# Performance work log

Hardware: AMD Instinct MI355X
Metric: run time of the kernel (lower is better)

The kernel has to match this reference:

```python
import jax, jax.numpy as jnp
import numpy as np

DIM = 768
HEADS = 16
DIM_HEAD = DIM // HEADS
SCALE = DIM_HEAD ** -0.5


def setup_inputs() -> dict:
    key = jax.random.key(0)
    k1, k2, k3, k4 = jax.random.split(key, 4)
    B, N = 8, 1024
    x = jax.random.normal(k1, (B, N, DIM), dtype=jnp.float32)
    # nn.Linear(dim, 3*dim, bias=False): stored so that qkv = x @ Wqkv
    Wqkv = jax.random.normal(k2, (DIM, 3 * DIM), dtype=jnp.float32) * (DIM ** -0.5)
    Wo = jax.random.normal(k3, (DIM, DIM), dtype=jnp.float32) * (DIM ** -0.5)
    bo = jax.random.normal(k4, (DIM,), dtype=jnp.float32) * 0.01
    return {"x": x, "Wqkv": Wqkv, "Wo": Wo, "bo": bo}


def reference(x, Wqkv, Wo, bo):
    B, N, _ = x.shape
    qkv = x @ Wqkv                                   # [B, N, 3*dim]
    # Faithful to torch: qkv.view(3, B, h, N, dim_head) — raw memory reshape
    qkv = jnp.reshape(qkv, (3, B, HEADS, N, DIM_HEAD))
    q, k, v = qkv[0], qkv[1], qkv[2]                 # each [B, h, N, dh]
    attn = jnp.einsum('bhnd,bhmd->bhnm', q, k) * SCALE   # [B, h, N, N]
    weight = jax.nn.softmax(attn, axis=-1)
    context = jnp.einsum('bhnm,bhmd->bhnd', weight, v)   # [B, h, N, dh]
    # Faithful to torch: context.view(B, -1, dim) — raw memory reshape
    concat = jnp.reshape(context, (B, N, DIM))
    return concat @ Wo + bo                          # dropout is identity at eval
```

## Files before the change

### kernel.cpp

```cpp
#include <hip/hip_runtime.h>
#include <hip/hip_bf16.h>

typedef __bf16 bf16x8 __attribute__((ext_vector_type(8)));
typedef __bf16 bf16x4 __attribute__((ext_vector_type(4)));
typedef float  f32x4  __attribute__((ext_vector_type(4)));

#define C2LOG 0.20823509f

__device__ __forceinline__ void gload_lds16(const __bf16* g, __bf16* l) {
    __builtin_amdgcn_global_load_lds(
        (const __attribute__((address_space(1))) void*)g,
        (__attribute__((address_space(3))) void*)l,
        16, 0, 0);
}

__global__ __launch_bounds__(256)
void prepass_kernel(const float* __restrict__ x, const float* __restrict__ Wqkv,
                    const float* __restrict__ Wo, __bf16* __restrict__ Xbf,
                    __bf16* __restrict__ WqkvT, __bf16* __restrict__ WoT) {
    __shared__ float tile[32][33];
    const int bx = blockIdx.x, t = threadIdx.x;
    if (bx < 6144) {
        const int i = (bx * 256 + t) * 4;
        float4 v = *(const float4*)&x[i];
        bf16x4 o;
        o[0] = (__bf16)v.x; o[1] = (__bf16)v.y; o[2] = (__bf16)v.z; o[3] = (__bf16)v.w;
        *(bf16x4*)&Xbf[i] = o;
        return;
    }
    const float* in; __bf16* out; int R, C, bxx;
    if (bx < 6144 + 1728) { bxx = bx - 6144; in = Wqkv; out = WqkvT; R = 768; C = 2304;
        const int c0 = (bxx % 72) * 32, r0 = (bxx / 72) * 32;
        const int tx = t & 31, ty = t >> 5;
#pragma unroll
        for (int i = 0; i < 4; ++i)
            tile[ty + i * 8][tx] = in[(size_t)(r0 + ty + i * 8) * C + c0 + tx];
        __syncthreads();
#pragma unroll
        for (int i = 0; i < 4; ++i)
            out[(size_t)(c0 + ty + i * 8) * R + r0 + tx] = (__bf16)tile[tx][ty + i * 8];
    } else { bxx = bx - 6144 - 1728; in = Wo; out = WoT; R = 768; C = 768;
        const int c0 = (bxx % 24) * 32, r0 = (bxx / 24) * 32;
        const int tx = t & 31, ty = t >> 5;
#pragma unroll
        for (int i = 0; i < 4; ++i)
            tile[ty + i * 8][tx] = in[(size_t)(r0 + ty + i * 8) * C + c0 + tx];
        __syncthreads();
#pragma unroll
        for (int i = 0; i < 4; ++i)
            out[(size_t)(c0 + ty + i * 8) * R + r0 + tx] = (__bf16)tile[tx][ty + i * 8];
    }
}

__global__ __launch_bounds__(256, 3)
void gemm_bt_kernel(const __bf16* __restrict__ A, const __bf16* __restrict__ B,
                    __bf16* __restrict__ C, int M, int N, int K) {
    __shared__ __bf16 sA[128 * 64];
    __shared__ __bf16 sB[128 * 64];

    const int m0 = blockIdx.y * 128;
    const int n0 = blockIdx.x * 128;
    const int t = threadIdx.x;
    const int w = t >> 6, lane = t & 63;
    const int quad = lane >> 4, l15 = lane & 15;
    const int wm = w >> 1, wn = w & 1;

    int aRow[4], aKc[4];
#pragma unroll
    for (int b = 0; b < 4; ++b) {
        const int L = b * 256 + t;
        aRow[b] = L >> 3;
        aKc[b] = (L & 7) ^ (aRow[b] & 7);
    }

    f32x4 acc[4][4] = {};

    for (int k0 = 0; k0 < K; k0 += 64) {
#pragma unroll
        for (int b = 0; b < 4; ++b) {
            const int ldsOff = (b * 256 + w * 64) * 8;
            gload_lds16(A + (size_t)(m0 + aRow[b]) * K + k0 + aKc[b] * 8, &sA[ldsOff]);
            gload_lds16(B + (size_t)(n0 + aRow[b]) * K + k0 + aKc[b] * 8, &sB[ldsOff]);
        }
        __syncthreads();

#pragma unroll
        for (int ks = 0; ks < 2; ++ks) {
            bf16x8 aF[4], bF[4];
            const int slot = ((ks * 4 + quad) ^ (l15 & 7)) * 8;
#pragma unroll
            for (int mt = 0; mt < 4; ++mt)
                aF[mt] = *(const bf16x8*)&sA[(wm * 64 + mt * 16 + l15) * 64 + slot];
#pragma unroll
            for (int nt = 0; nt < 4; ++nt)
                bF[nt] = *(const bf16x8*)&sB[(wn * 64 + nt * 16 + l15) * 64 + slot];
#pragma unroll
            for (int mt = 0; mt < 4; ++mt)
#pragma unroll
                for (int nt = 0; nt < 4; ++nt)
                    acc[mt][nt] = __builtin_amdgcn_mfma_f32_16x16x32_bf16(aF[mt], bF[nt], acc[mt][nt], 0, 0, 0);
        }
        __syncthreads();
    }

#pragma unroll
    for (int nt = 0; nt < 4; ++nt) {
        const int col = n0 + wn * 64 + nt * 16 + l15;
#pragma unroll
        for (int mt = 0; mt < 4; ++mt)
#pragma unroll
            for (int r = 0; r < 4; ++r) {
                const int row = m0 + wm * 64 + mt * 16 + quad * 4 + r;
                C[(size_t)row * N + col] = (__bf16)acc[mt][nt][r];
            }
    }
}

__global__ __launch_bounds__(256, 4)
void gemm_bt64_kernel(const __bf16* __restrict__ A, const __bf16* __restrict__ B,
                      float* __restrict__ C, const float* __restrict__ bias,
                      int M, int N, int K) {
    __shared__ __bf16 sA[128 * 64];
    __shared__ __bf16 sB[64 * 64];

    const int m0 = blockIdx.y * 128;
    const int n0 = blockIdx.x * 64;
    const int t = threadIdx.x;
    const int w = t >> 6, lane = t & 63;
    const int quad = lane >> 4, l15 = lane & 15;

    int sRow[4], sKc[4];
#pragma unroll
    for (int b = 0; b < 4; ++b) {
        const int L = b * 256 + t;
        sRow[b] = L >> 3;
        sKc[b] = (L & 7) ^ (sRow[b] & 7);
    }

    f32x4 acc[2][4] = {};

    for (int k0 = 0; k0 < K; k0 += 64) {
#pragma unroll
        for (int b = 0; b < 4; ++b)
            gload_lds16(A + (size_t)(m0 + sRow[b]) * K + k0 + sKc[b] * 8,
                        &sA[(b * 256 + w * 64) * 8]);
#pragma unroll
        for (int b = 0; b < 2; ++b)
            gload_lds16(B + (size_t)(n0 + sRow[b]) * K + k0 + sKc[b] * 8,
                        &sB[(b * 256 + w * 64) * 8]);
        __syncthreads();

#pragma unroll
        for (int ks = 0; ks < 2; ++ks) {
            bf16x8 aF[2], bF[4];
            const int slot = ((ks * 4 + quad) ^ (l15 & 7)) * 8;
#pragma unroll
            for (int mt = 0; mt < 2; ++mt)
                aF[mt] = *(const bf16x8*)&sA[(w * 32 + mt * 16 + l15) * 64 + slot];
#pragma unroll
            for (int nt = 0; nt < 4; ++nt)
                bF[nt] = *(const bf16x8*)&sB[(nt * 16 + l15) * 64 + slot];
#pragma unroll
            for (int mt = 0; mt < 2; ++mt)
#pragma unroll
                for (int nt = 0; nt < 4; ++nt)
                    acc[mt][nt] = __builtin_amdgcn_mfma_f32_16x16x32_bf16(aF[mt], bF[nt], acc[mt][nt], 0, 0, 0);
        }
        __syncthreads();
    }

#pragma unroll
    for (int nt = 0; nt < 4; ++nt) {
        const int col = n0 + nt * 16 + l15;
        const float bv = bias[col];
#pragma unroll
        for (int mt = 0; mt < 2; ++mt)
#pragma unroll
            for (int r = 0; r < 4; ++r) {
                const int row = m0 + w * 32 + mt * 16 + quad * 4 + r;
                C[(size_t)row * N + col] = acc[mt][nt][r] + bv;
            }
    }
}

#define VT_STRIDE 132
#define P_STRIDE  132

__global__ __launch_bounds__(512, 4)
void attn_kernel(const __bf16* __restrict__ Y1, __bf16* __restrict__ Ctx) {
    __shared__ __bf16 Kl[128 * 64];
    __shared__ __bf16 Vt[48 * VT_STRIDE];
    __shared__ __bf16 Pl[128 * P_STRIDE];

    const int bx = blockIdx.x;
    const int bh = bx & 127, qt = bx >> 7;
    const int t = threadIdx.x, w = t >> 6, lane = t & 63;
    const int quad = lane >> 4, l15 = lane & 15;

    const size_t qBase = (size_t)bh * 49152;
    const size_t kBase = 6291456 + qBase;
    const size_t vBase = 12582912 + qBase;

    bf16x8 qf0, qf1;
    {
        const int row = qt * 128 + w * 16 + l15;
        qf0 = *(const bf16x8*)(Y1 + qBase + (size_t)row * 48 + quad * 8);
        if (quad < 2)
            qf1 = *(const bf16x8*)(Y1 + qBase + (size_t)row * 48 + 32 + quad * 8);
        else
            qf1 = bf16x8{};
    }

    const int kr0 = t >> 3, kd0 = t & 7;
    const int kr1 = (t + 512) >> 3, kd1 = (t + 512) & 7;
    int vkp[3], vdb[3], vkk[3];
#pragma unroll
    for (int c = 0; c < 3; ++c) {
        const int u = t + c * 512;
        vkp[c] = u & 127;
        vdb[c] = (u >> 7) * 4;
        vkk[c] = (vkp[c] >> 3) + ((vkp[c] & 7) << 4);
    }

    bf16x8 kreg0 = *(const bf16x8*)(Y1 + kBase + (size_t)kr0 * 48 + kd0 * 8);
    bf16x8 kreg1 = *(const bf16x8*)(Y1 + kBase + (size_t)kr1 * 48 + kd1 * 8);
    bf16x4 vreg[3];
#pragma unroll
    for (int c = 0; c < 3; ++c)
        vreg[c] = *(const bf16x4*)(Y1 + vBase + (size_t)vkk[c] * 48 + vdb[c]);

    f32x4 o[3] = {};
    float l_lane[4] = {0.f, 0.f, 0.f, 0.f};

    for (int it = 0; it < 8; ++it) {
        __syncthreads();

        *(bf16x8*)&Kl[kr0 * 64 + ((kd0 ^ (kr0 & 7)) << 3)] = kreg0;
        *(bf16x8*)&Kl[kr1 * 64 + ((kd1 ^ (kr1 & 7)) << 3)] = kreg1;
#pragma unroll
        for (int c = 0; c < 3; ++c)
#pragma unroll
            for (int j = 0; j < 4; ++j)
                Vt[(vdb[c] + j) * VT_STRIDE + vkp[c]] = vreg[c][j];

        if (it < 7) {
            const int kv1 = (it + 1) * 128;
            kreg0 = *(const bf16x8*)(Y1 + kBase + (size_t)(kv1 + kr0) * 48 + kd0 * 8);
            kreg1 = *(const bf16x8*)(Y1 + kBase + (size_t)(kv1 + kr1) * 48 + kd1 * 8);
#pragma unroll
            for (int c = 0; c < 3; ++c)
                vreg[c] = *(const bf16x4*)(Y1 + vBase + (size_t)(kv1 + vkk[c]) * 48 + vdb[c]);
        }

        __syncthreads();

        f32x4 s[8];
#pragma unroll
        for (int nt = 0; nt < 8; ++nt) {
            const int krow = nt * 16 + l15;
            const int base = krow * 64;
            bf16x8 kf0 = *(const bf16x8*)&Kl[base + ((quad ^ (krow & 7)) << 3)];
            bf16x8 kf1 = *(const bf16x8*)&Kl[base + (((4 + quad) ^ (krow & 7)) << 3)];
            f32x4 z = {};
            z = __builtin_amdgcn_mfma_f32_16x16x32_bf16(qf0, kf0, z, 0, 0, 0);
            s[nt] = __builtin_amdgcn_mfma_f32_16x16x32_bf16(qf1, kf1, z, 0, 0, 0);
        }

#pragma unroll
        for (int r = 0; r < 4; ++r) {
            bf16x8 pk;
            float ls = 0.f;
#pragma unroll
            for (int nt = 0; nt < 8; ++nt) {
                float p = __builtin_amdgcn_exp2f(s[nt][r] * C2LOG);
                ls += p;
                pk[nt] = (__bf16)p;
            }
            l_lane[r] += ls;
            *(bf16x8*)&Pl[(w * 16 + quad * 4 + r) * P_STRIDE + l15 * 8] = pk;
        }

        bf16x8 pa[4];
#pragma unroll
        for (int ks = 0; ks < 4; ++ks)
            pa[ks] = *(const bf16x8*)&Pl[(w * 16 + l15) * P_STRIDE + ks * 32 + quad * 8];
#pragma unroll
        for (int nt = 0; nt < 3; ++nt) {
#pragma unroll
            for (int ks = 0; ks < 4; ++ks) {
                bf16x8 vb = *(const bf16x8*)&Vt[(nt * 16 + l15) * VT_STRIDE + ks * 32 + quad * 8];
                o[nt] = __builtin_amdgcn_mfma_f32_16x16x32_bf16(pa[ks], vb, o[nt], 0, 0, 0);
            }
        }
    }

    float inv[4];
#pragma unroll
    for (int r = 0; r < 4; ++r) {
        float ls = l_lane[r];
#pragma unroll
        for (int off = 1; off < 16; off <<= 1)
            ls += __shfl_xor(ls, off);
        inv[r] = __builtin_amdgcn_rcpf(ls);
    }

    __syncthreads();
    __bf16* Ob = Vt;
#pragma unroll
    for (int nt = 0; nt < 3; ++nt) {
        const int d = nt * 16 + l15;
#pragma unroll
        for (int r = 0; r < 4; ++r)
            Ob[(w * 16 + quad * 4 + r) * 48 + d] = (__bf16)(o[nt][r] * inv[r]);
    }
    __syncthreads();
    __bf16* dst = Ctx + qBase + (size_t)qt * 128 * 48;
    *(bf16x8*)(dst + t * 8) = *(const bf16x8*)&Ob[t * 8];
    if (t < 256)
        *(bf16x8*)(dst + (t + 512) * 8) = *(const bf16x8*)&Ob[(t + 512) * 8];
}

extern "C" void kernel_launch(void* const* d_in, const int* in_sizes, int n_in,
                              void* d_out, int out_size, void* d_ws, size_t ws_size,
                              hipStream_t stream) {
    const float* x    = (const float*)d_in[0];
    const float* Wqkv = (const float*)d_in[1];
    const float* Wo   = (const float*)d_in[2];
    const float* bo   = (const float*)d_in[3];
    float* out = (float*)d_out;

    char* ws = (char*)d_ws;
    __bf16* Xbf    = (__bf16*)(ws + 0);
    __bf16* WqkvT  = (__bf16*)(ws + 12582912);
    __bf16* WoT    = (__bf16*)(ws + 16121856);
    __bf16* Y1     = (__bf16*)(ws + 17301504);
    __bf16* Ctx    = (__bf16*)(ws + 55050240);

    prepass_kernel<<<8448, 256, 0, stream>>>(x, Wqkv, Wo, Xbf, WqkvT, WoT);

    gemm_bt_kernel<<<dim3(18, 64), 256, 0, stream>>>(Xbf, WqkvT, Y1, 8192, 2304, 768);

    attn_kernel<<<1024, 512, 0, stream>>>(Y1, Ctx);

    gemm_bt64_kernel<<<dim3(12, 64), 256, 0, stream>>>(Ctx, WoT, out, bo, 8192, 768, 768);
}
```

Before: 199.8 us.

## Enlarge QKV GEMM tile to 256x128 and prescale Q by softmax constant

The QKV projection GEMM now uses 512-thread blocks covering 256 rows by 128 columns. The B tile is shared across eight waves instead of four, which is meant to reduce global and LDS traffic per output. Separately, the attention kernel multiplies Q by the scaled log2e constant once at load, so the per-element multiply before exp2 in the softmax loop goes away. Rounding scaled Q to bf16 adds a little precision error, and the larger GEMM tile halves the grid and lowers occupancy.

```diff
diff --git a/kernel.cpp b/kernel.cpp
--- a/kernel.cpp
+++ b/kernel.cpp
@@ -52,36 +52,38 @@
     }
 }
 
-__global__ __launch_bounds__(256, 3)
+__global__ __launch_bounds__(512, 2)
 void gemm_bt_kernel(const __bf16* __restrict__ A, const __bf16* __restrict__ B,
                     __bf16* __restrict__ C, int M, int N, int K) {
-    __shared__ __bf16 sA[128 * 64];
+    __shared__ __bf16 sA[256 * 64];
     __shared__ __bf16 sB[128 * 64];
 
-    const int m0 = blockIdx.y * 128;
+    const int m0 = blockIdx.y * 256;
     const int n0 = blockIdx.x * 128;
     const int t = threadIdx.x;
     const int w = t >> 6, lane = t & 63;
     const int quad = lane >> 4, l15 = lane & 15;
     const int wm = w >> 1, wn = w & 1;
 
-    int aRow[4], aKc[4];
+    int sRow[4], sKc[4];
 #pragma unroll
     for (int b = 0; b < 4; ++b) {
-        const int L = b * 256 + t;
-        aRow[b] = L >> 3;
-        aKc[b] = (L & 7) ^ (aRow[b] & 7);
+        const int L = b * 512 + t;
+        sRow[b] = L >> 3;
+        sKc[b] = (L & 7) ^ (sRow[b] & 7);
     }
 
     f32x4 acc[4][4] = {};
 
     for (int k0 = 0; k0 < K; k0 += 64) {
 #pragma unroll
-        for (int b = 0; b < 4; ++b) {
-            const int ldsOff = (b * 256 + w * 64) * 8;
-            gload_lds16(A + (size_t)(m0 + aRow[b]) * K + k0 + aKc[b] * 8, &sA[ldsOff]);
-            gload_lds16(B + (size_t)(n0 + aRow[b]) * K + k0 + aKc[b] * 8, &sB[ldsOff]);
-        }
+        for (int b = 0; b < 4; ++b)
+            gload_lds16(A + (size_t)(m0 + sRow[b]) * K + k0 + sKc[b] * 8,
+                        &sA[(b * 512 + w * 64) * 8]);
+#pragma unroll
+        for (int b = 0; b < 2; ++b)
+            gload_lds16(B + (size_t)(n0 + sRow[b]) * K + k0 + sKc[b] * 8,
+                        &sB[(b * 512 + w * 64) * 8]);
         __syncthreads();
 
 #pragma unroll
@@ -204,11 +206,16 @@
     bf16x8 qf0, qf1;
     {
         const int row = qt * 128 + w * 16 + l15;
-        qf0 = *(const bf16x8*)(Y1 + qBase + (size_t)row * 48 + quad * 8);
-        if (quad < 2)
-            qf1 = *(const bf16x8*)(Y1 + qBase + (size_t)row * 48 + 32 + quad * 8);
-        else
-            qf1 = bf16x8{};
+        bf16x8 a = *(const bf16x8*)(Y1 + qBase + (size_t)row * 48 + quad * 8);
+#pragma unroll
+        for (int j = 0; j < 8; ++j) a[j] = (__bf16)((float)a[j] * C2LOG);
+        qf0 = a;
+        if (quad < 2) {
+            bf16x8 b = *(const bf16x8*)(Y1 + qBase + (size_t)row * 48 + 32 + quad * 8);
+#pragma unroll
+            for (int j = 0; j < 8; ++j) b[j] = (__bf16)((float)b[j] * C2LOG);
+            qf1 = b;
+        } else qf1 = bf16x8{};
     }
 
     const int kr0 = t >> 3, kd0 = t & 7;
@@ -272,7 +279,7 @@
             float ls = 0.f;
 #pragma unroll
             for (int nt = 0; nt < 8; ++nt) {
-                float p = __builtin_amdgcn_exp2f(s[nt][r] * C2LOG);
+                float p = __builtin_amdgcn_exp2f(s[nt][r]);
                 ls += p;
                 pk[nt] = (__bf16)p;
             }
@@ -338,7 +345,7 @@
 
     prepass_kernel<<<8448, 256, 0, stream>>>(x, Wqkv, Wo, Xbf, WqkvT, WoT);
 
-    gemm_bt_kernel<<<dim3(18, 64), 256, 0, stream>>>(Xbf, WqkvT, Y1, 8192, 2304, 768);
+    gemm_bt_kernel<<<dim3(18, 32), 512, 0, stream>>>(Xbf, WqkvT, Y1, 8192, 2304, 768);
 
     attn_kernel<<<1024, 512, 0, stream>>>(Y1, Ctx);
 
```

Result: no change. 199.5 us (-0.2%).
